# Optimization experiments

Hardware: AMD Instinct MI355X
Metric: run time of the kernel (lower is better)

The kernel has to match this reference:

```python
import jax, jax.numpy as jnp
import numpy as np

D_MODEL = 1024
N_HEADS = 16
CHUNK = 64
EPS = 1e-6


def elu_plus_1(x):
    return jax.nn.elu(x) + 1.0


def setup_inputs() -> dict:
    key = jax.random.key(0)
    kx, kq, kk, kv, ko = jax.random.split(key, 5)
    B, T = 4, 4096
    # xavier_uniform for square (D, D) weights: limit = sqrt(6/(D+D))
    lim = float(np.sqrt(6.0 / (D_MODEL + D_MODEL)))
    mk = lambda k: jax.random.uniform(k, (D_MODEL, D_MODEL), jnp.float32, -lim, lim)
    return {
        "x": jax.random.normal(kx, (B, T, D_MODEL), jnp.float32),
        "W_q": mk(kq),
        "W_k": mk(kk),
        "W_v": mk(kv),
        "W_o": mk(ko),
    }


def reference(x, W_q, W_k, W_v, W_o):
    B, T, D = x.shape
    H = N_HEADS
    dk = D // H
    dv = dk
    C = CHUNK
    N = T // C  # T chosen divisible by chunk size (no padding needed)

    q = (x @ W_q.T).reshape(B, T, H, dk)
    k = (x @ W_k.T).reshape(B, T, H, dk)
    v = (x @ W_v.T).reshape(B, T, H, dv)

    phi_q = elu_plus_1(q).reshape(B, N, C, H, dk)
    phi_k = elu_plus_1(k).reshape(B, N, C, H, dk)
    vc = v.reshape(B, N, C, H, dv)

    # Per-chunk key-value outer products and key sums, then exclusive prefix
    # sums over chunks give the carried state S and normalizer z at each
    # chunk's start (same math as the sequential chunk loop).
    KV = jnp.einsum('bnchk,bnchv->bnhkv', phi_k, vc)      # (B,N,H,dk,dv)
    Ksum = phi_k.sum(axis=2)                               # (B,N,C->sum,H,dk) -> (B,N,H,dk)
    KV_cum = jnp.cumsum(KV, axis=1)
    Ksum_cum = jnp.cumsum(Ksum, axis=1)
    S_prefix = jnp.concatenate([jnp.zeros_like(KV_cum[:, :1]), KV_cum[:, :-1]], axis=1)
    z_prefix = jnp.concatenate([jnp.zeros_like(Ksum_cum[:, :1]), Ksum_cum[:, :-1]], axis=1)

    # Inter-chunk contribution from carried state
    inter = jnp.einsum('bnchk,bnhkv->bnchv', phi_q, S_prefix)   # (B,N,C,H,dv)
    z_inter = jnp.einsum('bnchk,bnhk->bnch', phi_q, z_prefix)   # (B,N,C,H)

    # Intra-chunk causal attention
    mask = jnp.tril(jnp.ones((C, C), dtype=x.dtype))
    attn = jnp.einsum('bnihk,bnjhk->bnhij', phi_q, phi_k) * mask  # (B,N,H,C,C)
    intra = jnp.einsum('bnhij,bnjhv->bnihv', attn, vc)            # (B,N,C,H,dv)
    z_intra = attn.sum(axis=-1).transpose(0, 1, 3, 2)             # (B,N,C,H)

    denom = jnp.clip((z_inter + z_intra)[..., None], 1e-6, None)
    y = (inter + intra) / denom                                   # (B,N,C,H,dv)
    y = y.reshape(B, T, H * dv)
    return y @ W_o.T
```

## Files before the change

kernel.cpp:

```cpp
#include <hip/hip_runtime.h>


typedef unsigned short u16;
typedef float  f32x4 __attribute__((ext_vector_type(4)));
typedef short  b16x8 __attribute__((ext_vector_type(8)));
typedef u16    u16x4 __attribute__((ext_vector_type(4)));
typedef u16    u16x8 __attribute__((ext_vector_type(8)));

#define DEVINL __device__ __forceinline__

DEVINL u16 f2b(float f) {
  unsigned u = __float_as_uint(f);
  return (u16)((u + 0x7fffu + ((u >> 16) & 1u)) >> 16);
}
DEVINL float b2f(u16 s) { return __uint_as_float(((unsigned)s) << 16); }

DEVINL f32x4 mfma16(b16x8 a, b16x8 b, f32x4 c) {
  return __builtin_amdgcn_mfma_f32_16x16x32_bf16(a, b, c, 0, 0, 0);
}

DEVINL float phi_elu1(float v) { return v > 0.f ? v + 1.f : __expf(v); }

__global__ void cvt_kernel(const float* __restrict__ in, u16* __restrict__ out, int n8) {
  int stride = gridDim.x * blockDim.x;
  for (int i = blockIdx.x * blockDim.x + threadIdx.x; i < n8; i += stride) {
    const float* p = in + (size_t)i * 8;
    f32x4 a = *(const f32x4*)p;
    f32x4 b = *(const f32x4*)(p + 4);
    u16x8 o;
    o[0] = f2b(a[0]); o[1] = f2b(a[1]); o[2] = f2b(a[2]); o[3] = f2b(a[3]);
    o[4] = f2b(b[0]); o[5] = f2b(b[1]); o[6] = f2b(b[2]); o[7] = f2b(b[3]);
    *(u16x8*)(out + (size_t)i * 8) = o;
  }
}

__global__ void cvt4_kernel(const float* __restrict__ p0, const float* __restrict__ p1,
                            const float* __restrict__ p2, const float* __restrict__ p3,
                            u16* __restrict__ o0, u16* __restrict__ o1,
                            u16* __restrict__ o2, u16* __restrict__ o3) {
  const float* in; u16* out;
  switch (blockIdx.y) {
    case 0: in = p0; out = o0; break;
    case 1: in = p1; out = o1; break;
    case 2: in = p2; out = o2; break;
    default: in = p3; out = o3; break;
  }
  int i = blockIdx.x * blockDim.x + threadIdx.x;
  const float* p = in + (size_t)i * 8;
  f32x4 a = *(const f32x4*)p;
  f32x4 b = *(const f32x4*)(p + 4);
  u16x8 o;
  o[0] = f2b(a[0]); o[1] = f2b(a[1]); o[2] = f2b(a[2]); o[3] = f2b(a[3]);
  o[4] = f2b(b[0]); o[5] = f2b(b[1]); o[6] = f2b(b[2]); o[7] = f2b(b[3]);
  *(u16x8*)(out + (size_t)i * 8) = o;
}

#define GEMM_SETUP                                                              \
  __shared__ char lds[131072];                                                  \
  const int tid = threadIdx.x, wid = tid >> 6, l = tid & 63;                    \
  const int l15 = l & 15, lg = l >> 4;                                          \
  const int wr = wid >> 2, wc = wid & 3;                                        \
  const int ntn = N >> 8;                                                       \
  const int nwg = gridDim.x, bid = blockIdx.x;                                  \
  const int cpx = nwg >> 3;                                                     \
  const int sb = (bid & 7) * cpx + (bid >> 3);                                  \
  const int tm = sb / ntn, tn = sb - tm * ntn;                                  \
  const int colX0 = (lg * 16) ^ ((l15 & 7) << 4);                               \
  const int colX1 = (64 + lg * 16) ^ ((l15 & 7) << 4);                          \
  char* ldsA = lds + wr * 16384 + l15 * 128;                                    \
  char* ldsB = lds + 32768 + (wc >> 1) * 16384 + ((wc & 1) * 64 + l15) * 128;   \
  const int srow = tid >> 3;                                                    \
  const int scol = ((((tid & 7) * 16) ^ ((srow & 7) << 4)) >> 1);               \
  const u16* sA = A + (size_t)(tm * 256 + srow) * 1024 + scol;                  \
  const u16* sB = B + (size_t)(tn * 256 + srow) * 1024 + scol;                  \
  char* ldsStage = lds + wid * 1024;

#define STAGE(tt, h)                                                            \
  do {                                                                          \
    const u16* s_ = ((h) < 2 ? sA : sB) + (size_t)(((h) & 1) * 128) * 1024 +    \
                    (size_t)(tt) * 64;                                          \
    char* d_ = ldsStage + (((tt) & 1) << 16) + ((h) < 2 ? 0 : 32768) +          \
               (((h) & 1) << 14);                                               \
    __builtin_amdgcn_global_load_lds(                                           \
        (const __attribute__((address_space(1))) void*)(s_),                    \
        (__attribute__((address_space(3))) void*)(d_), 16, 0, 0);               \
    __builtin_amdgcn_global_load_lds(                                           \
        (const __attribute__((address_space(1))) void*)(s_ + 64 * 1024),        \
        (__attribute__((address_space(3))) void*)(d_ + 8192), 16, 0, 0);        \
  } while (0)

#define BAR_SB()                                                                \
  do {                                                                          \
    __builtin_amdgcn_s_barrier();                                               \
    __builtin_amdgcn_sched_barrier(0);                                          \
  } while (0)

#define GEMM_EPILOGUE                                                           \
  _Pragma("unroll") for (int fm = 0; fm < 8; ++fm)                              \
    _Pragma("unroll") for (int fn = 0; fn < 4; ++fn)                            \
      _Pragma("unroll") for (int r = 0; r < 4; ++r) {                           \
        size_t grow = (size_t)tm * 256 + wr * 128 + fm * 16 + lg * 4 + r;       \
        size_t gcol = (size_t)tn * 256 + wc * 64 + fn * 16 + l15;               \
        float v = acc[fm][fn][r];                                               \
        if (PHI) v = phi_elu1(v);                                               \
        OT* p = C + grow * (size_t)N + gcol;                                    \
        if constexpr (sizeof(OT) == 2) *p = (OT)f2b(v);                         \
        else                           *p = (OT)v;                              \
      }

template <bool PHI, typename OT>
__global__ __launch_bounds__(512, 2) void gemm256g(const u16* __restrict__ A,
                                                   const u16* __restrict__ B,
                                                   OT* __restrict__ C, int M, int N) {
  GEMM_SETUP

  f32x4 acc[8][4];
#pragma unroll
  for (int i = 0; i < 8; i++)
#pragma unroll
    for (int j = 0; j < 4; j++) acc[i][j] = f32x4{0.f, 0.f, 0.f, 0.f};

  STAGE(0, 0); STAGE(0, 1); STAGE(0, 2); STAGE(0, 3);
  STAGE(1, 2); STAGE(1, 3);
  asm volatile("s_waitcnt vmcnt(4)" ::: "memory");

  b16x8 a0[4], a1[4], b0[4], b1[4];
  for (int t = 0; t < 16; ++t) {
    const int cb = (t & 1) << 16;
    BAR_SB();
#pragma unroll
    for (int fm = 0; fm < 4; fm++) {
      a0[fm] = *(const b16x8*)(ldsA + cb + fm * 2048 + colX0);
      a1[fm] = *(const b16x8*)(ldsA + cb + (4 + fm) * 2048 + colX0);
    }
#pragma unroll
    for (int fn = 0; fn < 4; fn++) b0[fn] = *(const b16x8*)(ldsB + cb + fn * 2048 + colX0);
    if (t < 15) { STAGE(t + 1, 0); STAGE(t + 1, 1); }
    __builtin_amdgcn_s_setprio(1);
#pragma unroll
    for (int fm = 0; fm < 4; fm++)
#pragma unroll
      for (int fn = 0; fn < 4; fn++) acc[fm][fn] = mfma16(a0[fm], b0[fn], acc[fm][fn]);
#pragma unroll
    for (int fm = 0; fm < 4; fm++)
#pragma unroll
      for (int fn = 0; fn < 4; fn++) acc[4 + fm][fn] = mfma16(a1[fm], b0[fn], acc[4 + fm][fn]);
    __builtin_amdgcn_s_setprio(0);
    BAR_SB();
#pragma unroll
    for (int fm = 0; fm < 4; fm++) {
      a0[fm] = *(const b16x8*)(ldsA + cb + fm * 2048 + colX1);
      a1[fm] = *(const b16x8*)(ldsA + cb + (4 + fm) * 2048 + colX1);
    }
#pragma unroll
    for (int fn = 0; fn < 4; fn++) b1[fn] = *(const b16x8*)(ldsB + cb + fn * 2048 + colX1);
    if (t < 14) { STAGE(t + 2, 2); STAGE(t + 2, 3); }
    __builtin_amdgcn_s_setprio(1);
#pragma unroll
    for (int fm = 0; fm < 4; fm++)
#pragma unroll
      for (int fn = 0; fn < 4; fn++) acc[fm][fn] = mfma16(a0[fm], b1[fn], acc[fm][fn]);
#pragma unroll
    for (int fm = 0; fm < 4; fm++)
#pragma unroll
      for (int fn = 0; fn < 4; fn++) acc[4 + fm][fn] = mfma16(a1[fm], b1[fn], acc[4 + fm][fn]);
    __builtin_amdgcn_s_setprio(0);
    if (t < 14) asm volatile("s_waitcnt vmcnt(4)" ::: "memory");
    else        asm volatile("s_waitcnt vmcnt(0)" ::: "memory");
  }

  GEMM_EPILOGUE
}

__global__ __launch_bounds__(256, 2) void kv_kernel(const u16* __restrict__ phiK,
                                                    const u16* __restrict__ vT,
                                                    u16* __restrict__ KVT,
                                                    float* __restrict__ Ksum) {
  __shared__ u16 tile[4][64][68];
  const int tid = threadIdx.x, wid = tid >> 6, l = tid & 63, l15 = l & 15, lg = l >> 4;
  const int bid = blockIdx.x, hg = bid & 3, bn = bid >> 2, n = bn & 63, b = bn >> 6;
  const int h = hg * 4 + wid;
  const size_t row0 = (size_t)b * 4096 + n * 64;
  const int dcol = h * 64;
  const size_t cb = (size_t)b * 4096 + n * 64 + lg * 8;

  b16x8 af[4][2];
#pragma unroll
  for (int fm = 0; fm < 4; fm++)
#pragma unroll
    for (int ks = 0; ks < 2; ks++)
      af[fm][ks] = *(const b16x8*)(vT + (size_t)(h * 64 + fm * 16 + l15) * 16384 + cb + ks * 32);

  u16 (*tw)[68] = tile[wid];
#pragma unroll
  for (int i = 0; i < 8; i++) {
    int tok = i * 8 + (l >> 3);
    int c8 = (l & 7) * 8;
    u16x8 v = *(const u16x8*)(phiK + (row0 + tok) * 1024 + dcol + c8);
    *(u16x4*)(&tw[tok][c8]) = u16x4{v[0], v[1], v[2], v[3]};
    *(u16x4*)(&tw[tok][c8 + 4]) = u16x4{v[4], v[5], v[6], v[7]};
  }
  __syncthreads();

  b16x8 bf[4][2];
#pragma unroll
  for (int fn = 0; fn < 4; fn++)
#pragma unroll
    for (int ks = 0; ks < 2; ks++) {
      b16x8 t;
#pragma unroll
      for (int j = 0; j < 8; j++)
        t[j] = (short)tw[lg * 8 + ks * 32 + j][fn * 16 + l15];
      bf[fn][ks] = t;
    }

  f32x4 acc[4][4];
#pragma unroll
  for (int i = 0; i < 4; i++)
#pragma unroll
    for (int j = 0; j < 4; j++) acc[i][j] = f32x4{0.f, 0.f, 0.f, 0.f};
#pragma unroll
  for (int ks = 0; ks < 2; ks++)
#pragma unroll
    for (int fm = 0; fm < 4; fm++)
#pragma unroll
      for (int fn = 0; fn < 4; fn++) acc[fm][fn] = mfma16(af[fm][ks], bf[fn][ks], acc[fm][fn]);

  float ksum[4] = {0.f, 0.f, 0.f, 0.f};
#pragma unroll
  for (int fn = 0; fn < 4; fn++) {
#pragma unroll
    for (int ks = 0; ks < 2; ks++)
#pragma unroll
      for (int j = 0; j < 8; j++) ksum[fn] += b2f((u16)bf[fn][ks][j]);
    ksum[fn] += __shfl_xor(ksum[fn], 16);
    ksum[fn] += __shfl_xor(ksum[fn], 32);
  }
  const size_t ob = (size_t)(b * 16 + h) * 64 + n;
  if (l < 16) {
#pragma unroll
    for (int fn = 0; fn < 4; fn++) Ksum[ob * 64 + fn * 16 + l15] = ksum[fn];
  }
#pragma unroll
  for (int fm = 0; fm < 4; fm++)
#pragma unroll
    for (int fn = 0; fn < 4; fn++)
#pragma unroll
      for (int r = 0; r < 4; r++)
        KVT[ob * 4096 + (size_t)(fm * 16 + lg * 4 + r) * 64 + fn * 16 + l15] =
            f2b(acc[fm][fn][r]);
}

__global__ __launch_bounds__(256) void scan_s(const u16* __restrict__ KVT,
                                              u16* __restrict__ ST,
                                              const float* __restrict__ Ksum,
                                              float* __restrict__ zpre) {
  if (blockIdx.x >= 1024) {
    const int gi = (blockIdx.x - 1024) * 256 + threadIdx.x;
    const size_t bh = gi >> 6;
    const int dk = gi & 63;
    float acc = 0.f;
    for (int n = 0; n < 64; n++) {
      size_t idx = (bh * 64 + n) * 64 + dk;
      zpre[idx] = acc;
      acc += Ksum[idx];
    }
    return;
  }
  const size_t base = (size_t)(blockIdx.x >> 4) * 64 * 4096 +
                      (blockIdx.x & 15) * 256 + threadIdx.x;
  float acc = 0.f;
  float v[4], w[4];
#pragma unroll
  for (int i = 0; i < 4; i++) v[i] = b2f(KVT[base + (size_t)i * 4096]);
  for (int n = 0; n < 64; n += 4) {
    if (n < 60) {
#pragma unroll
      for (int i = 0; i < 4; i++) w[i] = b2f(KVT[base + (size_t)(n + 4 + i) * 4096]);
    } else {
#pragma unroll
      for (int i = 0; i < 4; i++) w[i] = 0.f;
    }
#pragma unroll
    for (int i = 0; i < 4; i++) {
      ST[base + (size_t)(n + i) * 4096] = f2b(acc);
      acc += v[i];
    }
#pragma unroll
    for (int i = 0; i < 4; i++) v[i] = w[i];
  }
}

__global__ __launch_bounds__(256, 2) void attn_out(const u16* __restrict__ phiQ,
                                                   const u16* __restrict__ phiK,
                                                   const u16* __restrict__ vT,
                                                   const u16* __restrict__ ST,
                                                   const float* __restrict__ zpre,
                                                   u16* __restrict__ Y) {
  __shared__ char lds[4 * 8192 + 4 * 256];
  const int tid = threadIdx.x, wid = tid >> 6, l = tid & 63, l15 = l & 15, lg = l >> 4;
  const int bid = blockIdx.x, hg = bid & 3, bn = bid >> 2, n = bn & 63, b = bn >> 6;
  const int h = hg * 4 + wid;
  const size_t row0 = (size_t)b * 4096 + n * 64;
  const int dcol = h * 64;

  b16x8 qf[4][2];
#pragma unroll
  for (int fi = 0; fi < 4; fi++)
#pragma unroll
    for (int ks = 0; ks < 2; ks++)
      qf[fi][ks] = *(const b16x8*)(phiQ + (row0 + fi * 16 + l15) * 1024 + dcol + lg * 8 + ks * 32);

  f32x4 accT[4][4];
#pragma unroll
  for (int i = 0; i < 4; i++)
#pragma unroll
    for (int j = 0; j < 4; j++) accT[i][j] = f32x4{0.f, 0.f, 0.f, 0.f};
  {
    b16x8 kf[4][2];
#pragma unroll
    for (int fj = 0; fj < 4; fj++)
#pragma unroll
      for (int ks = 0; ks < 2; ks++)
        kf[fj][ks] = *(const b16x8*)(phiK + (row0 + fj * 16 + l15) * 1024 + dcol + lg * 8 + ks * 32);
#pragma unroll
    for (int ks = 0; ks < 2; ks++)
#pragma unroll
      for (int fj = 0; fj < 4; fj++)
#pragma unroll
        for (int fi = 0; fi < 4; fi++)
          accT[fj][fi] = mfma16(kf[fj][ks], qf[fi][ks], accT[fj][fi]);
  }

  const size_t zb = ((size_t)(b * 16 + h) * 64 + n) * 64;
  float zi[4] = {0.f, 0.f, 0.f, 0.f};
#pragma unroll
  for (int ks = 0; ks < 2; ks++) {
    f32x4 z0 = *(const f32x4*)(zpre + zb + lg * 8 + ks * 32);
    f32x4 z1 = *(const f32x4*)(zpre + zb + lg * 8 + ks * 32 + 4);
#pragma unroll
    for (int fi = 0; fi < 4; fi++)
#pragma unroll
      for (int j = 0; j < 4; j++) {
        zi[fi] += b2f((u16)qf[fi][ks][j])     * z0[j];
        zi[fi] += b2f((u16)qf[fi][ks][j + 4]) * z1[j];
      }
  }

  char* abuf = lds + wid * 8192;
  float zt[4] = {0.f, 0.f, 0.f, 0.f};
#pragma unroll
  for (int fi = 0; fi < 4; fi++) {
    const int i = fi * 16 + l15;
    const int swz = (i & 7) << 4;
#pragma unroll
    for (int fj = 0; fj < 4; fj++) {
      f32x4 v = accT[fj][fi];
#pragma unroll
      for (int r = 0; r < 4; r++) {
        int j = fj * 16 + lg * 4 + r;
        if (j > i) v[r] = 0.f;
        zt[fi] += v[r];
      }
      unsigned w0 = (unsigned)f2b(v[0]) | ((unsigned)f2b(v[1]) << 16);
      unsigned w1 = (unsigned)f2b(v[2]) | ((unsigned)f2b(v[3]) << 16);
      int jb = (fj * 16 + lg * 4) * 2;
      *(unsigned*)(abuf + i * 128 + (jb ^ swz)) = w0;
      *(unsigned*)(abuf + i * 128 + ((jb + 4) ^ swz)) = w1;
    }
  }

  float* dbuf = (float*)(lds + 32768 + wid * 256);
#pragma unroll
  for (int fi = 0; fi < 4; fi++) {
    float z = zi[fi] + zt[fi];
    z += __shfl_xor(z, 16);
    z += __shfl_xor(z, 32);
    float rd = 1.f / fmaxf(z, 1e-6f);
    if (l < 16) dbuf[fi * 16 + l15] = rd;
  }
  __syncthreads();

  b16x8 stf[4][2], vf[4][2];
  const size_t stb = ((size_t)(b * 16 + h) * 64 + n) * 4096;
#pragma unroll
  for (int fn = 0; fn < 4; fn++)
#pragma unroll
    for (int ks = 0; ks < 2; ks++) {
      stf[fn][ks] = *(const b16x8*)(ST + stb + (size_t)(fn * 16 + l15) * 64 + lg * 8 + ks * 32);
      vf[fn][ks]  = *(const b16x8*)(vT + (size_t)(dcol + fn * 16 + l15) * 16384 +
                                    (size_t)b * 4096 + n * 64 + lg * 8 + ks * 32);
    }
  f32x4 acc[4][4];
#pragma unroll
  for (int i = 0; i < 4; i++)
#pragma unroll
    for (int j = 0; j < 4; j++) acc[i][j] = f32x4{0.f, 0.f, 0.f, 0.f};
#pragma unroll
  for (int ks = 0; ks < 2; ks++)
#pragma unroll
    for (int fm = 0; fm < 4; fm++)
#pragma unroll
      for (int fn = 0; fn < 4; fn++) acc[fm][fn] = mfma16(qf[fm][ks], stf[fn][ks], acc[fm][fn]);
#pragma unroll
  for (int fm = 0; fm < 4; fm++) {
    const int i = fm * 16 + l15;
    const int swz = (i & 7) << 4;
#pragma unroll
    for (int ks = 0; ks < 2; ks++) {
      b16x8 af = *(const b16x8*)(abuf + i * 128 + ((ks * 64 + lg * 16) ^ swz));
#pragma unroll
      for (int fn = 0; fn < 4; fn++) acc[fm][fn] = mfma16(af, vf[fn][ks], acc[fm][fn]);
    }
  }

#pragma unroll
  for (int fm = 0; fm < 4; fm++)
#pragma unroll
    for (int r = 0; r < 4; r++) {
      float rd = dbuf[fm * 16 + lg * 4 + r];
#pragma unroll
      for (int fn = 0; fn < 4; fn++)
        Y[(row0 + fm * 16 + lg * 4 + r) * 1024 + dcol + fn * 16 + l15] =
            f2b(acc[fm][fn][r] * rd);
    }
}

extern "C" void kernel_launch(void* const* d_in, const int* in_sizes, int n_in,
                              void* d_out, int out_size, void* d_ws, size_t ws_size,
                              hipStream_t stream) {
  const float* x  = (const float*)d_in[0];
  const float* Wq = (const float*)d_in[1];
  const float* Wk = (const float*)d_in[2];
  const float* Wv = (const float*)d_in[3];
  const float* Wo = (const float*)d_in[4];
  float* out = (float*)d_out;

  char* ws = (char*)d_ws;
  size_t off = 0;
  auto alloc = [&](size_t bytes) -> char* {
    char* p = ws + off;
    off += (bytes + 255) & ~(size_t)255;
    return p;
  };
  u16*   xb   = (u16*)alloc(33554432);
  u16*   wqb  = (u16*)alloc(2097152);
  u16*   wkb  = (u16*)alloc(2097152);
  u16*   wvb  = (u16*)alloc(2097152);
  u16*   wob  = (u16*)alloc(2097152);
  u16*   phiQ = (u16*)alloc(33554432);
  u16*   phiK = (u16*)alloc(33554432);
  u16*   vT   = (u16*)alloc(33554432);
  u16*   KVT  = (u16*)alloc(33554432);
  float* Ksum = (float*)alloc(1048576);
  u16*   ST   = (u16*)alloc(33554432);
  float* zpre = (float*)alloc(1048576);
  u16*   y    = xb;

  cvt_kernel<<<2048, 256, 0, stream>>>(x, xb, 2097152);
  cvt4_kernel<<<dim3(512, 4), 256, 0, stream>>>(Wq, Wk, Wv, Wo, wqb, wkb, wvb, wob);

  gemm256g<true, u16><<<256, 512, 0, stream>>>(xb, wqb, phiQ, 16384, 1024);
  gemm256g<true, u16><<<256, 512, 0, stream>>>(xb, wkb, phiK, 16384, 1024);
  gemm256g<false, u16><<<256, 512, 0, stream>>>(wvb, xb, vT, 1024, 16384);

  kv_kernel<<<1024, 256, 0, stream>>>(phiK, vT, KVT, Ksum);
  scan_s<<<1040, 256, 0, stream>>>(KVT, ST, Ksum, zpre);
  attn_out<<<1024, 256, 0, stream>>>(phiQ, phiK, vT, ST, zpre, y);

  gemm256g<false, float><<<256, 512, 0, stream>>>(y, wob, out, 16384, 1024);
}
```

Before: 233.1 us.

## Fuse Q, K, V projection GEMMs into one launch over concatenated weights

Replaces three separate projection GEMM launches with a single 768-block kernel that reads a concatenated bf16 weight buffer and picks Q, K or V output by block index. The V branch swaps MFMA operands so it can write the transposed vT layout directly from the x-by-W product. The MFMA loops are also interleaved across the two A fragment groups. The aim is to cut launch overhead and tail effects between the three GEMMs and share x tiles in L2 across them, at the cost of a divergent branch and strided transposed stores for V.

Result: slower. 644.7 us (+176.6%).

```diff
diff --git a/kernel.cpp b/kernel.cpp
--- a/kernel.cpp
+++ b/kernel.cpp
@@ -54,26 +54,6 @@
   o[4] = f2b(b[0]); o[5] = f2b(b[1]); o[6] = f2b(b[2]); o[7] = f2b(b[3]);
   *(u16x8*)(out + (size_t)i * 8) = o;
 }
-
-#define GEMM_SETUP                                                              \
-  __shared__ char lds[131072];                                                  \
-  const int tid = threadIdx.x, wid = tid >> 6, l = tid & 63;                    \
-  const int l15 = l & 15, lg = l >> 4;                                          \
-  const int wr = wid >> 2, wc = wid & 3;                                        \
-  const int ntn = N >> 8;                                                       \
-  const int nwg = gridDim.x, bid = blockIdx.x;                                  \
-  const int cpx = nwg >> 3;                                                     \
-  const int sb = (bid & 7) * cpx + (bid >> 3);                                  \
-  const int tm = sb / ntn, tn = sb - tm * ntn;                                  \
-  const int colX0 = (lg * 16) ^ ((l15 & 7) << 4);                               \
-  const int colX1 = (64 + lg * 16) ^ ((l15 & 7) << 4);                          \
-  char* ldsA = lds + wr * 16384 + l15 * 128;                                    \
-  char* ldsB = lds + 32768 + (wc >> 1) * 16384 + ((wc & 1) * 64 + l15) * 128;   \
-  const int srow = tid >> 3;                                                    \
-  const int scol = ((((tid & 7) * 16) ^ ((srow & 7) << 4)) >> 1);               \
-  const u16* sA = A + (size_t)(tm * 256 + srow) * 1024 + scol;                  \
-  const u16* sB = B + (size_t)(tn * 256 + srow) * 1024 + scol;                  \
-  char* ldsStage = lds + wid * 1024;
 
 #define STAGE(tt, h)                                                            \
   do {                                                                          \
@@ -95,24 +75,152 @@
     __builtin_amdgcn_sched_barrier(0);                                          \
   } while (0)
 
-#define GEMM_EPILOGUE                                                           \
-  _Pragma("unroll") for (int fm = 0; fm < 8; ++fm)                              \
-    _Pragma("unroll") for (int fn = 0; fn < 4; ++fn)                            \
-      _Pragma("unroll") for (int r = 0; r < 4; ++r) {                           \
-        size_t grow = (size_t)tm * 256 + wr * 128 + fm * 16 + lg * 4 + r;       \
-        size_t gcol = (size_t)tn * 256 + wc * 64 + fn * 16 + l15;               \
-        float v = acc[fm][fn][r];                                               \
-        if (PHI) v = phi_elu1(v);                                               \
-        OT* p = C + grow * (size_t)N + gcol;                                    \
-        if constexpr (sizeof(OT) == 2) *p = (OT)f2b(v);                         \
-        else                           *p = (OT)v;                              \
-      }
+__global__ __launch_bounds__(512, 2) void gemm256qkv(const u16* __restrict__ A,
+                                                     const u16* __restrict__ W,
+                                                     u16* __restrict__ phiQ,
+                                                     u16* __restrict__ phiK,
+                                                     u16* __restrict__ vT) {
+  __shared__ char lds[131072];
+  const int tid = threadIdx.x, wid = tid >> 6, l = tid & 63;
+  const int l15 = l & 15, lg = l >> 4;
+  const int wr = wid >> 2, wc = wid & 3;
+  const int bid = blockIdx.x;
+  const int g = bid & 255, rep = bid >> 8;
+  const int s = (g & 7) * 32 + (g >> 3);
+  const int tm = s >> 2, tnl = s & 3;
+  const bool isV = (rep == 2);
+
+  const int colX0 = (lg * 16) ^ ((l15 & 7) << 4);
+  const int colX1 = (64 + lg * 16) ^ ((l15 & 7) << 4);
+  char* ldsA = lds + wr * 16384 + l15 * 128;
+  char* ldsB = lds + 32768 + (wc >> 1) * 16384 + ((wc & 1) * 64 + l15) * 128;
+  const int srow = tid >> 3;
+  const int scol = ((((tid & 7) * 16) ^ ((srow & 7) << 4)) >> 1);
+  const u16* sA = A + (size_t)(tm * 256 + srow) * 1024 + scol;
+  const u16* sB = W + (size_t)((rep * 4 + tnl) * 256 + srow) * 1024 + scol;
+  char* ldsStage = lds + wid * 1024;
+
+  f32x4 acc[8][4];
+#pragma unroll
+  for (int i = 0; i < 8; i++)
+#pragma unroll
+    for (int j = 0; j < 4; j++) acc[i][j] = f32x4{0.f, 0.f, 0.f, 0.f};
+
+  STAGE(0, 0); STAGE(0, 1); STAGE(0, 2); STAGE(0, 3);
+  STAGE(1, 2); STAGE(1, 3);
+  asm volatile("s_waitcnt vmcnt(4)" ::: "memory");
+
+  b16x8 a0[4], a1[4], b0[4], b1[4];
+  for (int t = 0; t < 16; ++t) {
+    const int cb = (t & 1) << 16;
+    BAR_SB();
+#pragma unroll
+    for (int fm = 0; fm < 4; fm++) {
+      a0[fm] = *(const b16x8*)(ldsA + cb + fm * 2048 + colX0);
+      a1[fm] = *(const b16x8*)(ldsA + cb + (4 + fm) * 2048 + colX0);
+    }
+#pragma unroll
+    for (int fn = 0; fn < 4; fn++) b0[fn] = *(const b16x8*)(ldsB + cb + fn * 2048 + colX0);
+    if (t < 15) { STAGE(t + 1, 0); STAGE(t + 1, 1); }
+    __builtin_amdgcn_s_setprio(1);
+    if (!isV) {
+#pragma unroll
+      for (int fm = 0; fm < 4; fm++)
+#pragma unroll
+        for (int fn = 0; fn < 4; fn++) {
+          acc[fm][fn] = mfma16(a0[fm], b0[fn], acc[fm][fn]);
+          acc[4 + fm][fn] = mfma16(a1[fm], b0[fn], acc[4 + fm][fn]);
+        }
+    } else {
+#pragma unroll
+      for (int fm = 0; fm < 4; fm++)
+#pragma unroll
+        for (int fn = 0; fn < 4; fn++) {
+          acc[fm][fn] = mfma16(b0[fn], a0[fm], acc[fm][fn]);
+          acc[4 + fm][fn] = mfma16(b0[fn], a1[fm], acc[4 + fm][fn]);
+        }
+    }
+    __builtin_amdgcn_s_setprio(0);
+    BAR_SB();
+#pragma unroll
+    for (int fm = 0; fm < 4; fm++) {
+      a0[fm] = *(const b16x8*)(ldsA + cb + fm * 2048 + colX1);
+      a1[fm] = *(const b16x8*)(ldsA + cb + (4 + fm) * 2048 + colX1);
+    }
+#pragma unroll
+    for (int fn = 0; fn < 4; fn++) b1[fn] = *(const b16x8*)(ldsB + cb + fn * 2048 + colX1);
+    if (t < 14) { STAGE(t + 2, 2); STAGE(t + 2, 3); }
+    __builtin_amdgcn_s_setprio(1);
+    if (!isV) {
+#pragma unroll
+      for (int fm = 0; fm < 4; fm++)
+#pragma unroll
+        for (int fn = 0; fn < 4; fn++) {
+          acc[fm][fn] = mfma16(a0[fm], b1[fn], acc[fm][fn]);
+          acc[4 + fm][fn] = mfma16(a1[fm], b1[fn], acc[4 + fm][fn]);
+        }
+    } else {
+#pragma unroll
+      for (int fm = 0; fm < 4; fm++)
+#pragma unroll
+        for (int fn = 0; fn < 4; fn++) {
+          acc[fm][fn] = mfma16(b1[fn], a0[fm], acc[fm][fn]);
+          acc[4 + fm][fn] = mfma16(b1[fn], a1[fm], acc[4 + fm][fn]);
+        }
+    }
+    __builtin_amdgcn_s_setprio(0);
+    if (t < 14) asm volatile("s_waitcnt vmcnt(4)" ::: "memory");
+    else        asm volatile("s_waitcnt vmcnt(0)" ::: "memory");
+  }
+
+  if (!isV) {
+    u16* Cc = (rep == 0) ? phiQ : phiK;
+#pragma unroll
+    for (int fm = 0; fm < 8; ++fm)
+#pragma unroll
+      for (int fn = 0; fn < 4; ++fn)
+#pragma unroll
+        for (int r = 0; r < 4; ++r) {
+          size_t grow = (size_t)tm * 256 + wr * 128 + fm * 16 + lg * 4 + r;
+          size_t gcol = (size_t)tnl * 256 + wc * 64 + fn * 16 + l15;
+          Cc[grow * 1024 + gcol] = f2b(phi_elu1(acc[fm][fn][r]));
+        }
+  } else {
+#pragma unroll
+    for (int fm = 0; fm < 8; ++fm)
+#pragma unroll
+      for (int fn = 0; fn < 4; ++fn)
+#pragma unroll
+        for (int r = 0; r < 4; ++r) {
+          size_t vrow = (size_t)tnl * 256 + wc * 64 + fn * 16 + lg * 4 + r;
+          size_t tok = (size_t)tm * 256 + wr * 128 + fm * 16 + l15;
+          vT[vrow * 16384 + tok] = f2b(acc[fm][fn][r]);
+        }
+  }
+}
 
 template <bool PHI, typename OT>
 __global__ __launch_bounds__(512, 2) void gemm256g(const u16* __restrict__ A,
                                                    const u16* __restrict__ B,
                                                    OT* __restrict__ C, int M, int N) {
-  GEMM_SETUP
+  __shared__ char lds[131072];
+  const int tid = threadIdx.x, wid = tid >> 6, l = tid & 63;
+  const int l15 = l & 15, lg = l >> 4;
+  const int wr = wid >> 2, wc = wid & 3;
+  const int ntn = N >> 8;
+  const int nwg = gridDim.x, bid = blockIdx.x;
+  const int cpx = nwg >> 3;
+  const int sb = (bid & 7) * cpx + (bid >> 3);
+  const int tm = sb / ntn, tn = sb - tm * ntn;
+  const int colX0 = (lg * 16) ^ ((l15 & 7) << 4);
+  const int colX1 = (64 + lg * 16) ^ ((l15 & 7) << 4);
+  char* ldsA = lds + wr * 16384 + l15 * 128;
+  char* ldsB = lds + 32768 + (wc >> 1) * 16384 + ((wc & 1) * 64 + l15) * 128;
+  const int srow = tid >> 3;
+  const int scol = ((((tid & 7) * 16) ^ ((srow & 7) << 4)) >> 1);
+  const u16* sA = A + (size_t)(tm * 256 + srow) * 1024 + scol;
+  const u16* sB = B + (size_t)(tn * 256 + srow) * 1024 + scol;
+  char* ldsStage = lds + wid * 1024;
 
   f32x4 acc[8][4];
 #pragma unroll
@@ -140,11 +248,10 @@
 #pragma unroll
     for (int fm = 0; fm < 4; fm++)
 #pragma unroll
-      for (int fn = 0; fn < 4; fn++) acc[fm][fn] = mfma16(a0[fm], b0[fn], acc[fm][fn]);
-#pragma unroll
-    for (int fm = 0; fm < 4; fm++)
-#pragma unroll
-      for (int fn = 0; fn < 4; fn++) acc[4 + fm][fn] = mfma16(a1[fm], b0[fn], acc[4 + fm][fn]);
+      for (int fn = 0; fn < 4; fn++) {
+        acc[fm][fn] = mfma16(a0[fm], b0[fn], acc[fm][fn]);
+        acc[4 + fm][fn] = mfma16(a1[fm], b0[fn], acc[4 + fm][fn]);
+      }
     __builtin_amdgcn_s_setprio(0);
     BAR_SB();
 #pragma unroll
@@ -159,17 +266,29 @@
 #pragma unroll
     for (int fm = 0; fm < 4; fm++)
 #pragma unroll
-      for (int fn = 0; fn < 4; fn++) acc[fm][fn] = mfma16(a0[fm], b1[fn], acc[fm][fn]);
-#pragma unroll
-    for (int fm = 0; fm < 4; fm++)
-#pragma unroll
-      for (int fn = 0; fn < 4; fn++) acc[4 + fm][fn] = mfma16(a1[fm], b1[fn], acc[4 + fm][fn]);
+      for (int fn = 0; fn < 4; fn++) {
+        acc[fm][fn] = mfma16(a0[fm], b1[fn], acc[fm][fn]);
+        acc[4 + fm][fn] = mfma16(a1[fm], b1[fn], acc[4 + fm][fn]);
+      }
     __builtin_amdgcn_s_setprio(0);
     if (t < 14) asm volatile("s_waitcnt vmcnt(4)" ::: "memory");
     else        asm volatile("s_waitcnt vmcnt(0)" ::: "memory");
   }
 
-  GEMM_EPILOGUE
+#pragma unroll
+  for (int fm = 0; fm < 8; ++fm)
+#pragma unroll
+    for (int fn = 0; fn < 4; ++fn)
+#pragma unroll
+      for (int r = 0; r < 4; ++r) {
+        size_t grow = (size_t)tm * 256 + wr * 128 + fm * 16 + lg * 4 + r;
+        size_t gcol = (size_t)tn * 256 + wc * 64 + fn * 16 + l15;
+        float v = acc[fm][fn][r];
+        if (PHI) v = phi_elu1(v);
+        OT* p = C + grow * (size_t)N + gcol;
+        if constexpr (sizeof(OT) == 2) *p = (OT)f2b(v);
+        else                           *p = (OT)v;
+      }
 }
 
 __global__ __launch_bounds__(256, 2) void kv_kernel(const u16* __restrict__ phiK,
@@ -444,9 +563,7 @@
     return p;
   };
   u16*   xb   = (u16*)alloc(33554432);
-  u16*   wqb  = (u16*)alloc(2097152);
-  u16*   wkb  = (u16*)alloc(2097152);
-  u16*   wvb  = (u16*)alloc(2097152);
+  u16*   wcat = (u16*)alloc(6291456);
   u16*   wob  = (u16*)alloc(2097152);
   u16*   phiQ = (u16*)alloc(33554432);
   u16*   phiK = (u16*)alloc(33554432);
@@ -458,11 +575,10 @@
   u16*   y    = xb;
 
   cvt_kernel<<<2048, 256, 0, stream>>>(x, xb, 2097152);
-  cvt4_kernel<<<dim3(512, 4), 256, 0, stream>>>(Wq, Wk, Wv, Wo, wqb, wkb, wvb, wob);
-
-  gemm256g<true, u16><<<256, 512, 0, stream>>>(xb, wqb, phiQ, 16384, 1024);
-  gemm256g<true, u16><<<256, 512, 0, stream>>>(xb, wkb, phiK, 16384, 1024);
-  gemm256g<false, u16><<<256, 512, 0, stream>>>(wvb, xb, vT, 1024, 16384);
+  cvt4_kernel<<<dim3(512, 4), 256, 0, stream>>>(
+      Wq, Wk, Wv, Wo, wcat, wcat + 1048576, wcat + 2097152, wob);
+
+  gemm256qkv<<<768, 512, 0, stream>>>(xb, wcat, phiQ, phiK, vT);
 
   kv_kernel<<<1024, 256, 0, stream>>>(phiK, vT, KVT, Ksum);
   scan_s<<<1040, 256, 0, stream>>>(KVT, ST, Ksum, zpre);
```
